# Kernel optimization log

Measured on AMD Instinct MI355X. Metric: run time of the kernel, lower is better.

The kernel has to match this reference:

```python
import jax, jax.numpy as jnp
import numpy as np

D_MODEL = 1024
D_STATE = 16
D_CONV = 4
EXPAND = 2
D_INNER = D_MODEL * EXPAND
B_SZ = 2
SEQ = 4096


def setup_inputs() -> dict:
    key = jax.random.key(0)
    ks = jax.random.split(key, 11)
    rn = lambda i, shape, scale=1.0: jax.random.normal(ks[i], shape, jnp.float32) * scale
    return {
        "x": rn(0, (B_SZ, SEQ, D_MODEL)),
        "W_in": rn(1, (D_MODEL, D_INNER), D_MODEL ** -0.5),
        "b_in": rn(2, (D_INNER,), 0.01),
        "conv_w": rn(3, (D_INNER, 1, D_CONV), 0.1),   # torch depthwise layout [out_ch, in_ch/groups=1, k]
        "conv_b": rn(4, (D_INNER,), 0.01),
        # A scaled so tanh(A) is contractive -> stable recurrence over 4096 steps
        "A": rn(5, (D_STATE, D_STATE), 0.1),
        "Bp": rn(6, (D_STATE,)),   # B parameter [d_state, 1] flattened
        "Cp": rn(7, (D_STATE,)),   # C parameter [1, d_state] flattened
        "Dp": rn(8, (1,)),
        "W_out": rn(9, (D_INNER, D_MODEL), D_INNER ** -0.5),
        "b_out": rn(10, (D_MODEL,), 0.01),
    }


def reference(x, W_in, b_in, conv_w, conv_b, A, Bp, Cp, Dp, W_out, b_out):
    Bsz, S, _ = x.shape
    d_inner = W_in.shape[1]
    # input projection
    u = x @ W_in + b_in                              # [B, S, d_inner]
    # causal depthwise conv (torch pads k-1 both sides then slices [:S])
    u = u.transpose(0, 2, 1)                         # [B, d_inner, S]
    u = jax.lax.conv_general_dilated(
        u, conv_w, window_strides=(1,), padding=[(D_CONV - 1, 0)],
        dimension_numbers=("NCH", "OIH", "NCH"),
        feature_group_count=d_inner) + conv_b[None, :, None]
    u = u.transpose(0, 2, 1)                         # [B, S, d_inner]
    # per-channel scalar SSM shared across channels: h_t = tanh(A) h_{t-1} + B u_t; y_t = C h_t + D u_t
    At = jnp.tanh(A)                                 # [ds, ds]
    def step(h, u_t):                                # h: [B, d_inner, ds], u_t: [B, d_inner]
        h = jnp.einsum("ij,bdj->bdi", At, h) + u_t[..., None] * Bp
        y = jnp.einsum("j,bdj->bd", Cp, h) + Dp[0] * u_t
        return h, y
    h0 = jnp.zeros((Bsz, d_inner, Bp.shape[0]), x.dtype)
    _, ys = jax.lax.scan(step, h0, u.transpose(1, 0, 2))  # ys: [S, B, d_inner]
    y = jax.nn.silu(ys.transpose(1, 0, 2))           # [B, S, d_inner]
    return y @ W_out + b_out                         # [B, S, d_model]
```

## Files before the change

### kernel.cpp

```cpp
#include <hip/hip_runtime.h>

typedef unsigned short u16;
typedef float  f32x4  __attribute__((ext_vector_type(4)));
typedef __bf16 bf16x8 __attribute__((ext_vector_type(8)));
typedef u16    u16x2  __attribute__((ext_vector_type(2)));
typedef u16    u16x4  __attribute__((ext_vector_type(4)));

#define D_MODEL 1024
#define D_INNER 2048
#define B_SZ    2
#define SEQ     4096
#define MROWS   (B_SZ * SEQ)
#define LTAPS   64
#define VROW    136

__device__ __forceinline__ u16 f2bf(float f) {
    return __builtin_bit_cast(u16, (__bf16)f);
}
__device__ __forceinline__ float bf2f(u16 h) {
    unsigned u = ((unsigned)h) << 16;
    return __builtin_bit_cast(float, u);
}

typedef __attribute__((address_space(1))) void gv_t;
typedef __attribute__((address_space(3))) void lv_t;
__device__ __forceinline__ void glds16(const u16* g, u16* l) {
    __builtin_amdgcn_global_load_lds((gv_t*)g, (lv_t*)l, 16, 0, 0);
}
#define WAIT_VM0   0x0F70
#define WAIT_LGKM0 0xC07F

__device__ __forceinline__ void transpose_tile(
    const float* __restrict__ in, u16* __restrict__ out,
    int R, int C, int c0, int r0, int tid, float (*tile)[33])
{
    const int tx = tid & 31, ty = tid >> 5;
    for (int k = 0; k < 32; k += 8)
        tile[ty + k][tx] = in[(size_t)(r0 + ty + k) * C + c0 + tx];
    __syncthreads();
    for (int k = 0; k < 32; k += 8)
        out[(size_t)(c0 + ty + k) * R + r0 + tx] = f2bf(tile[tx][ty + k]);
}

__global__ __launch_bounds__(256) void prep_kernel(
    const float* __restrict__ x, u16* __restrict__ xb,
    const float* __restrict__ Win, u16* __restrict__ WinT,
    const float* __restrict__ Wout, u16* __restrict__ WoutT,
    const float* __restrict__ A, const float* __restrict__ Bp,
    const float* __restrict__ Cp, const float* __restrict__ Dp,
    u16* __restrict__ Amat64)
{
    __shared__ float tile[32][33];
    __shared__ float fs[LTAPS];
    const int bx = blockIdx.x, tid = threadIdx.x;
    if (bx < 8192) {
        size_t i = ((size_t)bx * 256 + tid) * 4;
        f32x4 v = *(const f32x4*)(x + i);
        u16x4 o;
        o.x = f2bf(v.x); o.y = f2bf(v.y); o.z = f2bf(v.z); o.w = f2bf(v.w);
        *(u16x4*)(xb + i) = o;
    } else if (bx < 10240) {
        const int flat = bx - 8192;
        transpose_tile(Win, WinT, 1024, 2048,
                       (flat & 63) * 32, (flat >> 6) * 32, tid, tile);
    } else if (bx < 12288) {
        const int flat = bx - 10240;
        transpose_tile(Wout, WoutT, 2048, 1024,
                       (flat & 31) * 32, (flat >> 5) * 32, tid, tile);
    } else {
        if (tid < 64) {
            const int i = tid & 15;
            float Atr[16];
            for (int j = 0; j < 16; j++) Atr[j] = tanhf(A[i * 16 + j]);
            float p = Bp[i];
            const float c  = Cp[i];
            const float d0 = Dp[0];
            for (int t = 0; t < LTAPS; t++) {
                float fv = c * p;
                fv += __shfl_xor(fv, 1); fv += __shfl_xor(fv, 2);
                fv += __shfl_xor(fv, 4); fv += __shfl_xor(fv, 8);
                if (tid == 0) fs[t] = fv + (t == 0 ? d0 : 0.f);
                float n0 = 0.f, n1 = 0.f, n2 = 0.f, n3 = 0.f;
                #pragma unroll
                for (int j = 0; j < 4; j++) {
                    n0 = fmaf(Atr[j],      __shfl(p, j),      n0);
                    n1 = fmaf(Atr[j + 4],  __shfl(p, j + 4),  n1);
                    n2 = fmaf(Atr[j + 8],  __shfl(p, j + 8),  n2);
                    n3 = fmaf(Atr[j + 12], __shfl(p, j + 12), n3);
                }
                p = (n0 + n1) + (n2 + n3);
            }
        }
        __syncthreads();
        for (int idx = tid; idx < 64 * 128; idx += 256) {
            const int i = idx >> 7, j = idx & 127;
            const int tau = 64 + i - j;
            float v = (tau >= 0 && tau < LTAPS) ? fs[tau] : 0.f;
            Amat64[idx] = f2bf(v);
        }
    }
}

template <int MODE>
__global__ __launch_bounds__(256) void gemm_bt_kernel(
    const u16* __restrict__ A, const u16* __restrict__ BT,
    void* __restrict__ Cout, const float* __restrict__ bias,
    int M, int N, int K)
{
    __shared__ u16 As[128 * 32];
    __shared__ u16 Bs[128 * 32];
    const int tid = threadIdx.x, lane = tid & 63, wid = tid >> 6;
    const int nTiles = gridDim.x;
    const int bid = blockIdx.x + nTiles * blockIdx.y;
    const int xcd = bid & 7;
    const int loc = bid >> 3;
    const int mt  = xcd * (gridDim.y >> 3) + (loc & 7);
    const int nt  = loc >> 3;
    const int m0 = mt * 128, n0 = nt * 128;
    const int sr = wid * 32 + (lane >> 2);
    const int sc = (lane & 3) * 8;
    const u16* ga = A  + (size_t)(m0 + sr) * K + sc;
    const u16* gb = BT + (size_t)(n0 + sr) * K + sc;
    u16* la = As + wid * 1024;
    u16* lb = Bs + wid * 1024;
    const int wm = (wid & 1) * 64, wn = (wid >> 1) * 64;
    const int fr = lane & 15, fq = lane >> 4;
    f32x4 acc[4][4] = {};
    glds16(ga, la);
    glds16(ga + (size_t)16 * K, la + 512);
    glds16(gb, lb);
    glds16(gb + (size_t)16 * K, lb + 512);
    const int iters = K >> 5;
    for (int it = 0; it < iters; ++it) {
        __builtin_amdgcn_s_waitcnt(WAIT_VM0);
        __builtin_amdgcn_s_barrier();
        bf16x8 af[4], bfr[4];
        #pragma unroll
        for (int i = 0; i < 4; i++)
            af[i]  = *(const bf16x8*)(As + (wm + i * 16 + fr) * 32 + fq * 8);
        #pragma unroll
        for (int i = 0; i < 4; i++)
            bfr[i] = *(const bf16x8*)(Bs + (wn + i * 16 + fr) * 32 + fq * 8);
        asm volatile("" ::: "memory");
        __builtin_amdgcn_s_waitcnt(WAIT_LGKM0);
        __builtin_amdgcn_s_barrier();
        if (it + 1 < iters) {
            const int k0 = (it + 1) << 5;
            glds16(ga + k0, la);
            glds16(ga + k0 + (size_t)16 * K, la + 512);
            glds16(gb + k0, lb);
            glds16(gb + k0 + (size_t)16 * K, lb + 512);
        }
        #pragma unroll
        for (int mi = 0; mi < 4; mi++)
            #pragma unroll
            for (int ni = 0; ni < 4; ni++)
                acc[mi][ni] = __builtin_amdgcn_mfma_f32_16x16x32_bf16(
                    bfr[ni], af[mi], acc[mi][ni], 0, 0, 0);
    }
    for (int ni = 0; ni < 4; ni++) {
        const int colb = n0 + wn + ni * 16 + fq * 4;
        const f32x4 bv = *(const f32x4*)(bias + colb);
        for (int mi = 0; mi < 4; mi++) {
            const int row = m0 + wm + mi * 16 + fr;
            f32x4 v = acc[mi][ni];
            v.x += bv.x; v.y += bv.y; v.z += bv.z; v.w += bv.w;
            if constexpr (MODE == 0) {
                u16x4 o;
                o.x = f2bf(v.x); o.y = f2bf(v.y); o.z = f2bf(v.z); o.w = f2bf(v.w);
                *(u16x4*)((u16*)Cout + (size_t)row * N + colb) = o;
            } else {
                *(f32x4*)((float*)Cout + (size_t)row * N + colb) = v;
            }
        }
    }
}

__global__ __launch_bounds__(256) void conv_fir_mfma_kernel(
    const u16* __restrict__ u, const float* __restrict__ cw,
    const float* __restrict__ cb, const u16* __restrict__ Amat64,
    u16* __restrict__ Y)
{
    __shared__ u16 VT[128 * VROW];
    const int tid = threadIdx.x;
    const int c0 = blockIdx.x * 128, t0 = blockIdx.y * 64, b = blockIdx.z;
    {
        const int tx = tid & 63, ty = tid >> 6;
        const int cg = c0 + tx * 2;
        const f32x4 wA = *(const f32x4*)(cw + cg * 4);
        const f32x4 wB = *(const f32x4*)(cw + cg * 4 + 4);
        const float cb0 = cb[cg], cb1 = cb[cg + 1];
        const u16* ucol = u + (size_t)b * SEQ * D_INNER + cg;
        const int s0 = t0 - 64 + ty * 32;
        u16* vr0 = VT + (tx * 2)     * VROW + ty * 32;
        u16* vr1 = VT + (tx * 2 + 1) * VROW + ty * 32;
        if (t0 == 0 && ty < 2) {
            const u16x4 z = {0, 0, 0, 0};
            #pragma unroll
            for (int j = 0; j < 8; j++) {
                *(u16x4*)(vr0 + j * 4) = z;
                *(u16x4*)(vr1 + j * 4) = z;
            }
        } else {
            float am3 = 0.f, am2 = 0.f, am1 = 0.f;
            float bm3 = 0.f, bm2 = 0.f, bm1 = 0.f;
            if (s0 > 0) {
                u16x2 d3 = *(const u16x2*)(ucol + (size_t)(s0 - 3) * D_INNER);
                u16x2 d2 = *(const u16x2*)(ucol + (size_t)(s0 - 2) * D_INNER);
                u16x2 d1 = *(const u16x2*)(ucol + (size_t)(s0 - 1) * D_INNER);
                am3 = bf2f(d3.x); bm3 = bf2f(d3.y);
                am2 = bf2f(d2.x); bm2 = bf2f(d2.y);
                am1 = bf2f(d1.x); bm1 = bf2f(d1.y);
            }
            #pragma unroll 2
            for (int j = 0; j < 8; j++) {
                const u16* p = ucol + (size_t)(s0 + j * 4) * D_INNER;
                u16x2 r0 = *(const u16x2*)(p);
                u16x2 r1 = *(const u16x2*)(p + (size_t)D_INNER);
                u16x2 r2 = *(const u16x2*)(p + (size_t)2 * D_INNER);
                u16x2 r3 = *(const u16x2*)(p + (size_t)3 * D_INNER);
                float a0 = bf2f(r0.x), b0 = bf2f(r0.y);
                float a1 = bf2f(r1.x), b1 = bf2f(r1.y);
                float a2 = bf2f(r2.x), b2 = bf2f(r2.y);
                float a3 = bf2f(r3.x), b3 = bf2f(r3.y);
                u16x4 oa, ob;
                oa.x = f2bf(cb0 + wA.x * am3 + wA.y * am2 + wA.z * am1 + wA.w * a0);
                oa.y = f2bf(cb0 + wA.x * am2 + wA.y * am1 + wA.z * a0  + wA.w * a1);
                oa.z = f2bf(cb0 + wA.x * am1 + wA.y * a0  + wA.z * a1  + wA.w * a2);
                oa.w = f2bf(cb0 + wA.x * a0  + wA.y * a1  + wA.z * a2  + wA.w * a3);
                ob.x = f2bf(cb1 + wB.x * bm3 + wB.y * bm2 + wB.z * bm1 + wB.w * b0);
                ob.y = f2bf(cb1 + wB.x * bm2 + wB.y * bm1 + wB.z * b0  + wB.w * b1);
                ob.z = f2bf(cb1 + wB.x * bm1 + wB.y * b0  + wB.z * b1  + wB.w * b2);
                ob.w = f2bf(cb1 + wB.x * b0  + wB.y * b1  + wB.z * b2  + wB.w * b3);
                *(u16x4*)(vr0 + j * 4) = oa;
                *(u16x4*)(vr1 + j * 4) = ob;
                am3 = a1; am2 = a2; am1 = a3;
                bm3 = b1; bm2 = b2; bm1 = b3;
            }
        }
    }
    __syncthreads();
    const int lane = tid & 63, wid = tid >> 6;
    const int wm = (wid & 1) * 32, wn = (wid >> 1) * 64;
    const int fr = lane & 15, fq = lane >> 4;
    f32x4 acc[2][4] = {};
    #pragma unroll
    for (int kq = 0; kq < 4; kq++) {
        const int k0 = kq * 32;
        bf16x8 af[2], bfr[4];
        #pragma unroll
        for (int mi = 0; mi < 2; mi++)
            af[mi] = *(const bf16x8*)(Amat64 + (wm + mi * 16 + fr) * 128 + k0 + fq * 8);
        #pragma unroll
        for (int ni = 0; ni < 4; ni++)
            bfr[ni] = *(const bf16x8*)(VT + (wn + ni * 16 + fr) * VROW + k0 + fq * 8);
        #pragma unroll
        for (int mi = 0; mi < 2; mi++)
            #pragma unroll
            for (int ni = 0; ni < 4; ni++)
                acc[mi][ni] = __builtin_amdgcn_mfma_f32_16x16x32_bf16(
                    bfr[ni], af[mi], acc[mi][ni], 0, 0, 0);
    }
    #pragma unroll
    for (int ni = 0; ni < 4; ni++) {
        const int cbase = c0 + wn + ni * 16 + fq * 4;
        #pragma unroll
        for (int mi = 0; mi < 2; mi++) {
            const int trow = t0 + wm + mi * 16 + fr;
            f32x4 v = acc[mi][ni];
            u16x4 o;
            o.x = f2bf(v.x / (1.f + __expf(-v.x)));
            o.y = f2bf(v.y / (1.f + __expf(-v.y)));
            o.z = f2bf(v.z / (1.f + __expf(-v.z)));
            o.w = f2bf(v.w / (1.f + __expf(-v.w)));
            *(u16x4*)(Y + ((size_t)(b * SEQ + trow)) * D_INNER + cbase) = o;
        }
    }
}

extern "C" void kernel_launch(void* const* d_in, const int* in_sizes, int n_in,
                              void* d_out, int out_size, void* d_ws, size_t ws_size,
                              hipStream_t stream)
{
    const float* x    = (const float*)d_in[0];
    const float* Win  = (const float*)d_in[1];
    const float* bin  = (const float*)d_in[2];
    const float* cw   = (const float*)d_in[3];
    const float* cb   = (const float*)d_in[4];
    const float* A    = (const float*)d_in[5];
    const float* Bp   = (const float*)d_in[6];
    const float* Cp   = (const float*)d_in[7];
    const float* Dp   = (const float*)d_in[8];
    const float* Wout = (const float*)d_in[9];
    const float* bout = (const float*)d_in[10];
    float* out = (float*)d_out;

    char* ws = (char*)d_ws;
    u16* xb     = (u16*)(ws);
    u16* WinT   = (u16*)(ws + 16777216);
    u16* WoutT  = (u16*)(ws + 20971520);
    u16* u      = (u16*)(ws + 25165824);
    u16* Y      = (u16*)(ws + 58720256);
    u16* Amat64 = (u16*)(ws + 92274688);

    prep_kernel<<<12289, 256, 0, stream>>>(x, xb, Win, WinT, Wout, WoutT,
                                           A, Bp, Cp, Dp, Amat64);
    gemm_bt_kernel<0><<<dim3(16, 64), 256, 0, stream>>>(xb, WinT, u, bin,
                                                        MROWS, D_INNER, D_MODEL);
    conv_fir_mfma_kernel<<<dim3(16, 64, 2), 256, 0, stream>>>(u, cw, cb, Amat64, Y);
    gemm_bt_kernel<1><<<dim3(8, 64), 256, 0, stream>>>(Y, WoutT, out, bout,
                                                       MROWS, D_MODEL, D_INNER);
}
```

Baseline: 243.9 us.

## Replace GEMM kernel with 8-wave 256-tile double-buffered swizzled LDS pipeline

```diff
diff --git a/kernel.cpp b/kernel.cpp
--- a/kernel.cpp
+++ b/kernel.cpp
@@ -101,68 +101,150 @@
     }
 }
 
-template <int MODE>
-__global__ __launch_bounds__(256) void gemm_bt_kernel(
+template <int BM, int BN, int WM, int WN, int MODE>
+__global__ __launch_bounds__(512, 2) void gemm8_kernel(
     const u16* __restrict__ A, const u16* __restrict__ BT,
     void* __restrict__ Cout, const float* __restrict__ bias,
-    int M, int N, int K)
-{
-    __shared__ u16 As[128 * 32];
-    __shared__ u16 Bs[128 * 32];
+    int N, int K)
+{
+    constexpr int WTM = BM / WM, WTN = BN / WN;
+    constexpr int FM = WTM / 16, FN = WTN / 16;
+    constexpr int RS = (FM == 8) ? 2 : 1;
+    constexpr int MPP = FM / RS;
+    constexpr int LPA = (BM * 64) / 8192;
+    constexpr int LPB = (BN * 64) / 8192;
+    constexpr int LPT = 2 * (LPA + LPB);
+    constexpr int BUFE = (BM + BN) * 64;
+    constexpr int WVM_HALF = 0x0F70 | (LPT / 2);
+    constexpr int WVM_ZERO = 0x0F70;
+    static_assert(WM * WN == 8, "8 waves");
+    static_assert((BM * 64) % 8192 == 0 && (BN * 64) % 8192 == 0, "half size");
+
+    __shared__ __align__(16) u16 sm[2 * BUFE];
     const int tid = threadIdx.x, lane = tid & 63, wid = tid >> 6;
-    const int nTiles = gridDim.x;
-    const int bid = blockIdx.x + nTiles * blockIdx.y;
-    const int xcd = bid & 7;
-    const int loc = bid >> 3;
-    const int mt  = xcd * (gridDim.y >> 3) + (loc & 7);
-    const int nt  = loc >> 3;
-    const int m0 = mt * 128, n0 = nt * 128;
-    const int sr = wid * 32 + (lane >> 2);
-    const int sc = (lane & 3) * 8;
-    const u16* ga = A  + (size_t)(m0 + sr) * K + sc;
-    const u16* gb = BT + (size_t)(n0 + sr) * K + sc;
-    u16* la = As + wid * 1024;
-    u16* lb = Bs + wid * 1024;
-    const int wm = (wid & 1) * 64, wn = (wid >> 1) * 64;
+    const int bid = blockIdx.x;
+    const int xcd = bid & 7, loc = bid >> 3;
+    const int mt = xcd * 4 + (loc & 3), nt = loc >> 2;
+    const int m0 = mt * BM, n0 = nt * BN;
+    const int wm = wid & (WM - 1), wn = wid / WM;
     const int fr = lane & 15, fq = lane >> 4;
-    f32x4 acc[4][4] = {};
-    glds16(ga, la);
-    glds16(ga + (size_t)16 * K, la + 512);
-    glds16(gb, lb);
-    glds16(gb + (size_t)16 * K, lb + 512);
-    const int iters = K >> 5;
-    for (int it = 0; it < iters; ++it) {
-        __builtin_amdgcn_s_waitcnt(WAIT_VM0);
-        __builtin_amdgcn_s_barrier();
-        bf16x8 af[4], bfr[4];
-        #pragma unroll
-        for (int i = 0; i < 4; i++)
-            af[i]  = *(const bf16x8*)(As + (wm + i * 16 + fr) * 32 + fq * 8);
-        #pragma unroll
-        for (int i = 0; i < 4; i++)
-            bfr[i] = *(const bf16x8*)(Bs + (wn + i * 16 + fr) * 32 + fq * 8);
-        asm volatile("" ::: "memory");
-        __builtin_amdgcn_s_waitcnt(WAIT_LGKM0);
-        __builtin_amdgcn_s_barrier();
-        if (it + 1 < iters) {
-            const int k0 = (it + 1) << 5;
-            glds16(ga + k0, la);
-            glds16(ga + k0 + (size_t)16 * K, la + 512);
-            glds16(gb + k0, lb);
-            glds16(gb + k0 + (size_t)16 * K, lb + 512);
-        }
-        #pragma unroll
-        for (int mi = 0; mi < 4; mi++)
-            #pragma unroll
-            for (int ni = 0; ni < 4; ni++)
-                acc[mi][ni] = __builtin_amdgcn_mfma_f32_16x16x32_bf16(
-                    bfr[ni], af[mi], acc[mi][ni], 0, 0, 0);
-    }
-    for (int ni = 0; ni < 4; ni++) {
-        const int colb = n0 + wn + ni * 16 + fq * 4;
+
+    auto mkp = [&](const u16* G, int r0, int q) -> const u16* {
+        const int qq = q + lane * 16;
+        const int lin = qq ^ (((qq >> 7) & 7) << 4);
+        return G + (size_t)(r0 + (lin >> 6)) * K + ((lin & 63) >> 1);
+    };
+    const u16* pA0 = mkp(A, m0, wid * 1024);
+    const u16* pA1 = (LPA == 2) ? mkp(A, m0, wid * 1024 + 8192) : pA0;
+    const u16* pB0 = mkp(BT, n0, wid * 1024);
+    const u16* pB1 = (LPB == 2) ? mkp(BT, n0, wid * 1024 + 8192) : pB0;
+
+    auto issueA = [&](int t1, int h) {
+        u16* lb = sm + (t1 & 1) * BUFE + h * (BM * 32) + (wid << 9);
+        const int ko = t1 * 64 + h * 32;
+        glds16(pA0 + ko, lb);
+        if constexpr (LPA == 2) glds16(pA1 + ko, lb + 4096);
+    };
+    auto issueB = [&](int t1, int h) {
+        u16* lb = sm + (t1 & 1) * BUFE + BM * 64 + h * (BN * 32) + (wid << 9);
+        const int ko = t1 * 64 + h * 32;
+        glds16(pB0 + ko, lb);
+        if constexpr (LPB == 2) glds16(pB1 + ko, lb + 4096);
+    };
+
+    int aoff[2][MPP], boff[FN];
+    #pragma unroll
+    for (int rh = 0; rh < RS; ++rh)
+        #pragma unroll
+        for (int mi = 0; mi < MPP; ++mi) {
+            const int lin = (wm * WTM + rh * 64 + mi * 16 + fr) * 64 + fq * 16;
+            aoff[rh][mi] = (lin ^ (((lin >> 7) & 7) << 4)) >> 1;
+        }
+    #pragma unroll
+    for (int ni = 0; ni < FN; ++ni) {
+        const int lin = (wn * WTN + ni * 16 + fr) * 64 + fq * 16;
+        boff[ni] = (lin ^ (((lin >> 7) & 7) << 4)) >> 1;
+    }
+
+    f32x4 acc[FM][FN] = {};
+    bf16x8 af[MPP], bfr[FN];
+
+    issueA(0, 0); issueB(0, 0); issueA(0, 1); issueB(0, 1);
+
+    const int NTm1 = (K >> 6) - 1;
+
+#define GPHASE(DO_ISSUE, WIMM)                                               \
+  {                                                                          \
+    if (rh == 0) {                                                           \
+      asm volatile("" ::: "memory");                                         \
+      __builtin_amdgcn_s_waitcnt(WIMM);                                      \
+      __builtin_amdgcn_sched_barrier(0);                                     \
+      __builtin_amdgcn_s_barrier();                                          \
+      __builtin_amdgcn_sched_barrier(0);                                     \
+    }                                                                        \
+    const u16* ab_ = sm + (t & 1) * BUFE + ks * (BM * 32);                   \
+    const u16* bb_ = sm + (t & 1) * BUFE + BM * 64 + ks * (BN * 32);         \
+    _Pragma("unroll")                                                        \
+    for (int mi = 0; mi < MPP; ++mi)                                         \
+      af[mi] = *(const bf16x8*)(ab_ + aoff[rh][mi]);                         \
+    if (rh == 0) {                                                           \
+      _Pragma("unroll")                                                      \
+      for (int ni = 0; ni < FN; ++ni)                                        \
+        bfr[ni] = *(const bf16x8*)(bb_ + boff[ni]);                          \
+    }                                                                        \
+    if (DO_ISSUE) {                                                          \
+      if (RS == 2) {                                                         \
+        if (rh == 0) issueA(t + 1, ks); else issueB(t + 1, ks);              \
+      } else {                                                               \
+        issueA(t + 1, ks); issueB(t + 1, ks);                                \
+      }                                                                      \
+    }                                                                        \
+    asm volatile("" ::: "memory");                                           \
+    __builtin_amdgcn_s_waitcnt(WAIT_LGKM0);                                  \
+    __builtin_amdgcn_sched_barrier(0);                                       \
+    __builtin_amdgcn_s_setprio(1);                                           \
+    _Pragma("unroll")                                                        \
+    for (int mi = 0; mi < MPP; ++mi)                                         \
+      _Pragma("unroll")                                                      \
+      for (int ni = 0; ni < FN; ++ni)                                        \
+        acc[rh * MPP + mi][ni] = __builtin_amdgcn_mfma_f32_16x16x32_bf16(    \
+            bfr[ni], af[mi], acc[rh * MPP + mi][ni], 0, 0, 0);               \
+    __builtin_amdgcn_s_setprio(0);                                           \
+    __builtin_amdgcn_s_barrier();                                            \
+  }
+
+    #pragma unroll 1
+    for (int t = 0; t < NTm1; ++t) {
+        #pragma unroll
+        for (int ks = 0; ks < 2; ++ks)
+            #pragma unroll
+            for (int rh = 0; rh < RS; ++rh)
+                GPHASE(true, WVM_HALF)
+    }
+    {
+        const int t = NTm1;
+        {
+            const int ks = 0;
+            #pragma unroll
+            for (int rh = 0; rh < RS; ++rh)
+                GPHASE(false, WVM_HALF)
+        }
+        {
+            const int ks = 1;
+            #pragma unroll
+            for (int rh = 0; rh < RS; ++rh)
+                GPHASE(false, WVM_ZERO)
+        }
+    }
+#undef GPHASE
+
+    #pragma unroll
+    for (int ni = 0; ni < FN; ++ni) {
+        const int colb = n0 + wn * WTN + ni * 16 + fq * 4;
         const f32x4 bv = *(const f32x4*)(bias + colb);
-        for (int mi = 0; mi < 4; mi++) {
-            const int row = m0 + wm + mi * 16 + fr;
+        #pragma unroll
+        for (int mi = 0; mi < FM; ++mi) {
+            const int row = m0 + wm * WTM + mi * 16 + fr;
             f32x4 v = acc[mi][ni];
             v.x += bv.x; v.y += bv.y; v.z += bv.z; v.w += bv.w;
             if constexpr (MODE == 0) {
@@ -305,9 +387,9 @@
 
     prep_kernel<<<12289, 256, 0, stream>>>(x, xb, Win, WinT, Wout, WoutT,
                                            A, Bp, Cp, Dp, Amat64);
-    gemm_bt_kernel<0><<<dim3(16, 64), 256, 0, stream>>>(xb, WinT, u, bin,
-                                                        MROWS, D_INNER, D_MODEL);
+    gemm8_kernel<256, 256, 2, 4, 0><<<256, 512, 0, stream>>>(
+        xb, WinT, u, bin, D_INNER, D_MODEL);
     conv_fir_mfma_kernel<<<dim3(16, 64, 2), 256, 0, stream>>>(u, cw, cb, Amat64, Y);
-    gemm_bt_kernel<1><<<dim3(8, 64), 256, 0, stream>>>(Y, WoutT, out, bout,
-                                                       MROWS, D_MODEL, D_INNER);
-}
+    gemm8_kernel<256, 128, 4, 2, 1><<<256, 512, 0, stream>>>(
+        Y, WoutT, out, bout, D_MODEL, D_INNER);
+}
```

New measurement: 226.1 us. 7.3% less time.

## Replace GEMM with 4-stage pipelined 256x128-tile kernel using swizzled LDS

Applied to the files above, without the earlier changes.

```diff
diff --git a/kernel.cpp b/kernel.cpp
--- a/kernel.cpp
+++ b/kernel.cpp
@@ -27,7 +27,7 @@
 __device__ __forceinline__ void glds16(const u16* g, u16* l) {
     __builtin_amdgcn_global_load_lds((gv_t*)g, (lv_t*)l, 16, 0, 0);
 }
-#define WAIT_VM0   0x0F70
+#define WAIT_VM(n) (0x0F70 | (n))
 #define WAIT_LGKM0 0xC07F
 
 __device__ __forceinline__ void transpose_tile(
@@ -102,67 +102,101 @@
 }
 
 template <int MODE>
-__global__ __launch_bounds__(256) void gemm_bt_kernel(
+__global__ __launch_bounds__(512, 2) void gemm_p4_kernel(
     const u16* __restrict__ A, const u16* __restrict__ BT,
     void* __restrict__ Cout, const float* __restrict__ bias,
-    int M, int N, int K)
-{
-    __shared__ u16 As[128 * 32];
-    __shared__ u16 Bs[128 * 32];
-    const int tid = threadIdx.x, lane = tid & 63, wid = tid >> 6;
-    const int nTiles = gridDim.x;
-    const int bid = blockIdx.x + nTiles * blockIdx.y;
-    const int xcd = bid & 7;
-    const int loc = bid >> 3;
-    const int mt  = xcd * (gridDim.y >> 3) + (loc & 7);
-    const int nt  = loc >> 3;
-    const int m0 = mt * 128, n0 = nt * 128;
-    const int sr = wid * 32 + (lane >> 2);
-    const int sc = (lane & 3) * 8;
-    const u16* ga = A  + (size_t)(m0 + sr) * K + sc;
-    const u16* gb = BT + (size_t)(n0 + sr) * K + sc;
-    u16* la = As + wid * 1024;
-    u16* lb = Bs + wid * 1024;
-    const int wm = (wid & 1) * 64, wn = (wid >> 1) * 64;
+    int N, int K)
+{
+    constexpr int REGU = (256 + 128) * 32;
+    __shared__ __align__(16) u16 sm[4 * REGU];
+    const int tid = threadIdx.x, lane = tid & 63;
+    const int wid = tid >> 6;
+    const int bid = blockIdx.x;
+    const int xcd = bid & 7, loc = bid >> 3;
+    const int mt = xcd * 4 + (loc & 3), nt = loc >> 2;
+    const int m0 = mt * 256, n0 = nt * 128;
+    const int wm = wid & 3, wn = wid >> 2;
     const int fr = lane & 15, fq = lane >> 4;
+
+    auto mk = [&](const u16* G, int r0, int q) -> const u16* {
+        const int l = q ^ (((q >> 7) & 7) << 4);
+        return G + (size_t)(r0 + (l >> 6)) * K + ((l & 63) >> 1);
+    };
+    const u16* pA0 = mk(A, m0, tid * 16);
+    const u16* pA1 = mk(A, m0, tid * 16 + 8192);
+    const u16* pB0 = mk(BT, n0, tid * 16);
+
+    auto glds_half = [&](int p) {
+        u16* rb = sm + (p & 3) * REGU;
+        const int ko = p * 32;
+        glds16(pA0 + ko, rb + tid * 8);
+        glds16(pA1 + ko, rb + tid * 8 + 4096);
+        glds16(pB0 + ko, rb + 8192 + tid * 8);
+    };
+
+    int aoff[4], boff[4];
+    #pragma unroll
+    for (int i = 0; i < 4; ++i) {
+        const int la = (wm * 64 + i * 16 + fr) * 64 + fq * 16;
+        aoff[i] = (la ^ (((la >> 7) & 7) << 4)) >> 1;
+        const int lb = (wn * 64 + i * 16 + fr) * 64 + fq * 16;
+        boff[i] = ((lb ^ (((lb >> 7) & 7) << 4)) >> 1) + 8192;
+    }
+
     f32x4 acc[4][4] = {};
-    glds16(ga, la);
-    glds16(ga + (size_t)16 * K, la + 512);
-    glds16(gb, lb);
-    glds16(gb + (size_t)16 * K, lb + 512);
-    const int iters = K >> 5;
-    for (int it = 0; it < iters; ++it) {
-        __builtin_amdgcn_s_waitcnt(WAIT_VM0);
-        __builtin_amdgcn_s_barrier();
-        bf16x8 af[4], bfr[4];
-        #pragma unroll
-        for (int i = 0; i < 4; i++)
-            af[i]  = *(const bf16x8*)(As + (wm + i * 16 + fr) * 32 + fq * 8);
-        #pragma unroll
-        for (int i = 0; i < 4; i++)
-            bfr[i] = *(const bf16x8*)(Bs + (wn + i * 16 + fr) * 32 + fq * 8);
-        asm volatile("" ::: "memory");
-        __builtin_amdgcn_s_waitcnt(WAIT_LGKM0);
-        __builtin_amdgcn_s_barrier();
-        if (it + 1 < iters) {
-            const int k0 = (it + 1) << 5;
-            glds16(ga + k0, la);
-            glds16(ga + k0 + (size_t)16 * K, la + 512);
-            glds16(gb + k0, lb);
-            glds16(gb + k0 + (size_t)16 * K, lb + 512);
-        }
-        #pragma unroll
-        for (int mi = 0; mi < 4; mi++)
-            #pragma unroll
-            for (int ni = 0; ni < 4; ni++)
-                acc[mi][ni] = __builtin_amdgcn_mfma_f32_16x16x32_bf16(
-                    bfr[ni], af[mi], acc[mi][ni], 0, 0, 0);
-    }
-    for (int ni = 0; ni < 4; ni++) {
-        const int colb = n0 + wn + ni * 16 + fq * 4;
+    const int NPH = K >> 5;
+
+    glds_half(0); glds_half(1); glds_half(2);
+    asm volatile("" ::: "memory");
+    __builtin_amdgcn_s_waitcnt(WAIT_VM(6));
+    __builtin_amdgcn_sched_barrier(0);
+    __builtin_amdgcn_s_barrier();
+
+#define P4_PHASE(p, ISSUE, WVM, LAST)                                        \
+  {                                                                          \
+    const u16* rb_ = sm + ((p) & 3) * REGU;                                  \
+    bf16x8 af[4], bfr[4];                                                    \
+    _Pragma("unroll")                                                        \
+    for (int i = 0; i < 4; ++i) af[i]  = *(const bf16x8*)(rb_ + aoff[i]);    \
+    _Pragma("unroll")                                                        \
+    for (int i = 0; i < 4; ++i) bfr[i] = *(const bf16x8*)(rb_ + boff[i]);    \
+    if (ISSUE) glds_half((p) + 3);                                           \
+    asm volatile("" ::: "memory");                                           \
+    __builtin_amdgcn_sched_barrier(0);                                       \
+    __builtin_amdgcn_s_barrier();                                            \
+    __builtin_amdgcn_s_waitcnt(WAIT_LGKM0);                                  \
+    __builtin_amdgcn_sched_barrier(0);                                       \
+    __builtin_amdgcn_s_setprio(1);                                           \
+    _Pragma("unroll")                                                        \
+    for (int mi = 0; mi < 4; ++mi)                                           \
+      _Pragma("unroll")                                                      \
+      for (int ni = 0; ni < 4; ++ni)                                         \
+        acc[mi][ni] = __builtin_amdgcn_mfma_f32_16x16x32_bf16(               \
+            bfr[ni], af[mi], acc[mi][ni], 0, 0, 0);                          \
+    __builtin_amdgcn_s_setprio(0);                                           \
+    if (!(LAST)) {                                                           \
+      asm volatile("" ::: "memory");                                         \
+      __builtin_amdgcn_s_waitcnt(WAIT_VM(WVM));                              \
+      __builtin_amdgcn_sched_barrier(0);                                     \
+      __builtin_amdgcn_s_barrier();                                          \
+    }                                                                        \
+  }
+
+    #pragma unroll 1
+    for (int p = 0; p < NPH - 3; ++p)
+        P4_PHASE(p, true, 6, false)
+    P4_PHASE(NPH - 3, false, 3, false)
+    P4_PHASE(NPH - 2, false, 0, false)
+    P4_PHASE(NPH - 1, false, 0, true)
+#undef P4_PHASE
+
+    #pragma unroll
+    for (int ni = 0; ni < 4; ++ni) {
+        const int colb = n0 + wn * 64 + ni * 16 + fq * 4;
         const f32x4 bv = *(const f32x4*)(bias + colb);
-        for (int mi = 0; mi < 4; mi++) {
-            const int row = m0 + wm + mi * 16 + fr;
+        #pragma unroll
+        for (int mi = 0; mi < 4; ++mi) {
+            const int row = m0 + wm * 64 + mi * 16 + fr;
             f32x4 v = acc[mi][ni];
             v.x += bv.x; v.y += bv.y; v.z += bv.z; v.w += bv.w;
             if constexpr (MODE == 0) {
@@ -305,9 +339,9 @@
 
     prep_kernel<<<12289, 256, 0, stream>>>(x, xb, Win, WinT, Wout, WoutT,
                                            A, Bp, Cp, Dp, Amat64);
-    gemm_bt_kernel<0><<<dim3(16, 64), 256, 0, stream>>>(xb, WinT, u, bin,
-                                                        MROWS, D_INNER, D_MODEL);
+    gemm_p4_kernel<0><<<512, 512, 0, stream>>>(xb, WinT, u, bin,
+                                               D_INNER, D_MODEL);
     conv_fir_mfma_kernel<<<dim3(16, 64, 2), 256, 0, stream>>>(u, cw, cb, Amat64, Y);
-    gemm_bt_kernel<1><<<dim3(8, 64), 256, 0, stream>>>(Y, WoutT, out, bout,
-                                                       MROWS, D_MODEL, D_INNER);
-}
+    gemm_p4_kernel<1><<<256, 512, 0, stream>>>(Y, WoutT, out, bout,
+                                               D_MODEL, D_INNER);
+}
```

After: 247.7 us. Within noise of the previous version (+1.6%).
